# Optimization experiments

Measured on AMD Instinct MI355X. Metric: run time of the kernel, lower is better.

Reference implementation:

```python
import jax, jax.numpy as jnp
import numpy as np

N, E, D, H, DH = 10000, 160000, 1024, 4, 256  # nodes, edges, feat dim, heads, per-head dim
NB, G = 3, 64  # num_blocks, num graphs in batch
NEG_SLOPE = 0.2  # PyG GATConv default


def setup_inputs() -> dict:
    key = jax.random.key(0)
    ks = jax.random.split(key, 8)
    x = jax.random.normal(ks[0], (N, D), jnp.float32)
    edge_index = jax.random.randint(ks[1], (2, E), 0, N)
    batch = jnp.sort(jax.random.randint(ks[2], (N,), 0, G))
    W = jax.random.normal(ks[3], (NB, D, H * DH), jnp.float32) * 0.03
    a_src = jax.random.normal(ks[4], (NB, H, DH), jnp.float32) * 0.1
    a_dst = jax.random.normal(ks[5], (NB, H, DH), jnp.float32) * 0.1
    b = jnp.zeros((NB, H * DH), jnp.float32)
    Wr = jax.random.normal(ks[6], (D, 2), jnp.float32) * 0.03
    br = jnp.zeros((2,), jnp.float32)
    return dict(x=x, edge_index=edge_index, batch=batch, W=W, a_src=a_src,
                a_dst=a_dst, b=b, Wr=Wr, br=br)


def _gat_conv(x, src, dst, W, asrc, adst, bias):
    # Linear projection per head: [N, H, DH]
    h = (x @ W).reshape(N, H, DH)
    # Per-node attention logits (src/dst halves of the GAT attention vector)
    es = jnp.einsum('nhd,hd->nh', h, asrc)  # [N, H]
    ed = jnp.einsum('nhd,hd->nh', h, adst)  # [N, H]
    # Edge scores + LeakyReLU
    e = jax.nn.leaky_relu(es[src] + ed[dst], NEG_SLOPE)  # [Etot, H]
    # Segment softmax over edges sharing the same destination node
    m = jax.ops.segment_max(e, dst, num_segments=N)
    p = jnp.exp(e - m[dst])
    s = jax.ops.segment_sum(p, dst, num_segments=N)
    alpha = p / (s[dst] + 1e-16)  # [Etot, H]
    # Scatter-aggregate weighted source features
    out = jax.ops.segment_sum(h[src] * alpha[:, :, None], dst, num_segments=N)
    return out.reshape(N, H * DH) + bias


def reference(x, edge_index, batch, W, a_src, a_dst, b, Wr, br):
    # PyG GATConv adds self-loops by default
    loops = jnp.arange(N)
    src = jnp.concatenate([edge_index[0], loops])
    dst = jnp.concatenate([edge_index[1], loops])
    # Faithful to the source: each block reads the ORIGINAL x; dropout in eval mode.
    h = x
    for i in range(NB):
        h = jax.nn.relu(_gat_conv(x, src, dst, W[i], a_src[i], a_dst[i], b[i]))
    # global_mean_pool over graph assignment `batch`
    sums = jax.ops.segment_sum(h, batch, num_segments=G)
    cnt = jax.ops.segment_sum(jnp.ones((N, 1), h.dtype), batch, num_segments=G)
    pooled = sums / jnp.maximum(cnt, 1.0)
    return pooled @ Wr + br
```

## Files before the change

kernel.cpp:

```cpp
#include <hip/hip_runtime.h>
#include <hip/hip_bf16.h>

#define N_NODES 10000
#define N_EDGES 160000
#define ETOT    (N_NODES + N_EDGES)
#define DIM     1024
#define NHEAD   4
#define DHEAD   256
#define NGRAPH  64
#define NEG_SLOPE 0.2f

typedef short  bf16x8 __attribute__((ext_vector_type(8)));
typedef float  f32x4  __attribute__((ext_vector_type(4)));
typedef unsigned short u16x4 __attribute__((ext_vector_type(4)));

__device__ __forceinline__ unsigned short f2bf_rne(float v) {
    unsigned u = __builtin_bit_cast(unsigned, v);
    return (unsigned short)((u + 0x7fffu + ((u >> 16) & 1u)) >> 16);
}
__device__ __forceinline__ float bf2f(unsigned short b) {
    return __builtin_bit_cast(float, (unsigned)b << 16);
}
__device__ __forceinline__ float lrelu(float x) { return x > 0.f ? x : NEG_SLOPE * x; }

__global__ void zero_k(float* p, int n) {
    int i = blockIdx.x * 256 + threadIdx.x;
    if (i < n) p[i] = 0.f;
}

__global__ __launch_bounds__(256) void prep_x(const float* __restrict__ x,
                                              unsigned short* __restrict__ xhi,
                                              unsigned short* __restrict__ xlo) {
    int i = blockIdx.x * 256 + threadIdx.x;
    if ((size_t)i * 4 >= (size_t)N_NODES * DIM) return;
    f32x4 v = *(const f32x4*)(x + (size_t)i * 4);
    u16x4 hi, lo;
#pragma unroll
    for (int j = 0; j < 4; ++j) {
        unsigned short hb = f2bf_rne(v[j]);
        float r = v[j] - bf2f(hb);
        hi[j] = hb;
        lo[j] = f2bf_rne(r);
    }
    *(u16x4*)(xhi + (size_t)i * 4) = hi;
    *(u16x4*)(xlo + (size_t)i * 4) = lo;
}

__global__ __launch_bounds__(256) void prep_w(const float* __restrict__ W2,
                                              unsigned short* __restrict__ wthi,
                                              unsigned short* __restrict__ wtlo) {
    __shared__ float tile[64][65];
    int bc = blockIdx.x;
    int bk = blockIdx.y;
    int t = threadIdx.x;
    int tj = t & 63, ti = t >> 6;
#pragma unroll
    for (int u = 0; u < 16; ++u) {
        int r = u * 4 + ti;
        tile[r][tj] = W2[(size_t)(bk * 64 + r) * DIM + bc * 64 + tj];
    }
    __syncthreads();
#pragma unroll
    for (int u = 0; u < 16; ++u) {
        int cr = u * 4 + ti;
        float v = tile[tj][cr];
        unsigned short hb = f2bf_rne(v);
        float rres = v - bf2f(hb);
        size_t o = (size_t)(bc * 64 + cr) * DIM + bk * 64 + tj;
        wthi[o] = hb;
        wtlo[o] = f2bf_rne(rres);
    }
}

#define BM 128
#define BN 128
#define BK 32
#define LDK 40

__global__ __launch_bounds__(256) void gemm3(const unsigned short* __restrict__ xhi,
                                             const unsigned short* __restrict__ xlo,
                                             const unsigned short* __restrict__ wthi,
                                             const unsigned short* __restrict__ wtlo,
                                             float* __restrict__ hout) {
    __shared__ short lds[4][BM * LDK];
    const int t = threadIdx.x;
    const int r0 = blockIdx.y * BM;
    const int c0 = blockIdx.x * BN;
    const int lane = t & 63, wid = t >> 6;
    const int wm = wid >> 1, wn = wid & 1;

    f32x4 acc[4][4];
#pragma unroll
    for (int mi = 0; mi < 4; ++mi)
#pragma unroll
        for (int ni = 0; ni < 4; ++ni) acc[mi][ni] = (f32x4){0.f, 0.f, 0.f, 0.f};

    const int rL = lane & 15;
    const int koff = (lane >> 4) * 8;

    for (int k0 = 0; k0 < DIM; k0 += BK) {
        __syncthreads();
#pragma unroll
        for (int u = 0; u < 8; ++u) {
            int idx = u * 256 + t;
            int which = idx >> 9;
            int rem = idx & 511;
            int row = rem >> 2;
            int seg = rem & 3;
            const unsigned short* src;
            bool ok = true;
            if (which == 0)      { int gr = r0 + row; ok = gr < N_NODES; src = xhi + (size_t)gr * DIM + k0 + seg * 8; }
            else if (which == 1) { int gr = r0 + row; ok = gr < N_NODES; src = xlo + (size_t)gr * DIM + k0 + seg * 8; }
            else if (which == 2) { src = wthi + (size_t)(c0 + row) * DIM + k0 + seg * 8; }
            else                 { src = wtlo + (size_t)(c0 + row) * DIM + k0 + seg * 8; }
            bf16x8 v = {0,0,0,0,0,0,0,0};
            if (ok) v = *(const bf16x8*)src;
            *(bf16x8*)&lds[which][row * LDK + seg * 8] = v;
        }
        __syncthreads();

        bf16x8 ahi[4], alo[4], bhi[4], blo[4];
#pragma unroll
        for (int mi = 0; mi < 4; ++mi) {
            int row = wm * 64 + mi * 16 + rL;
            ahi[mi] = *(const bf16x8*)&lds[0][row * LDK + koff];
            alo[mi] = *(const bf16x8*)&lds[1][row * LDK + koff];
        }
#pragma unroll
        for (int ni = 0; ni < 4; ++ni) {
            int row = wn * 64 + ni * 16 + rL;
            bhi[ni] = *(const bf16x8*)&lds[2][row * LDK + koff];
            blo[ni] = *(const bf16x8*)&lds[3][row * LDK + koff];
        }
#pragma unroll
        for (int mi = 0; mi < 4; ++mi)
#pragma unroll
            for (int ni = 0; ni < 4; ++ni) {
                f32x4 c = acc[mi][ni];
                c = __builtin_amdgcn_mfma_f32_16x16x32_bf16(ahi[mi], bhi[ni], c, 0, 0, 0);
                c = __builtin_amdgcn_mfma_f32_16x16x32_bf16(ahi[mi], blo[ni], c, 0, 0, 0);
                c = __builtin_amdgcn_mfma_f32_16x16x32_bf16(alo[mi], bhi[ni], c, 0, 0, 0);
                acc[mi][ni] = c;
            }
    }

#pragma unroll
    for (int mi = 0; mi < 4; ++mi)
#pragma unroll
        for (int ni = 0; ni < 4; ++ni)
#pragma unroll
            for (int v = 0; v < 4; ++v) {
                int row = r0 + wm * 64 + mi * 16 + ((lane >> 4) << 2) + v;
                if (row < N_NODES) {
                    int col = c0 + wn * 64 + ni * 16 + (lane & 15);
                    hout[(size_t)row * DIM + col] = acc[mi][ni][v];
                }
            }
}

__global__ __launch_bounds__(256) void dots_k(const float* __restrict__ h,
                                              const float* __restrict__ asrc,
                                              const float* __restrict__ adst,
                                              float* __restrict__ es,
                                              float* __restrict__ ed) {
    int wid = threadIdx.x >> 6, lane = threadIdx.x & 63;
    int n = blockIdx.x * 4 + wid;
    if (n >= N_NODES) return;
    const float* hr = h + (size_t)n * DIM;
    f32x4 sa = {0.f, 0.f, 0.f, 0.f}, sd = {0.f, 0.f, 0.f, 0.f};
#pragma unroll
    for (int k = 0; k < 4; ++k)
#pragma unroll
        for (int j = 0; j < 4; ++j) {
            int col = k * 256 + j * 64 + lane;
            float v = hr[col];
            sa[k] += v * asrc[col];
            sd[k] += v * adst[col];
        }
#pragma unroll
    for (int d = 1; d < 64; d <<= 1) {
#pragma unroll
        for (int k = 0; k < 4; ++k) {
            sa[k] += __shfl_xor(sa[k], d);
            sd[k] += __shfl_xor(sd[k], d);
        }
    }
    if (lane == 0) {
        *(f32x4*)(es + (size_t)n * 4) = sa;
        *(f32x4*)(ed + (size_t)n * 4) = sd;
    }
}

__global__ void init_counts(const int* __restrict__ batch, int* cnt, int* cursor, int* gcnt) {
    int n = blockIdx.x * 256 + threadIdx.x;
    if (n >= N_NODES) return;
    cnt[n] = 1;
    cursor[n] = 0;
    atomicAdd(gcnt + batch[n], 1);
}

__global__ void edge_hist(const int* __restrict__ dst, int* cnt) {
    int e = blockIdx.x * 256 + threadIdx.x;
    if (e >= N_EDGES) return;
    atomicAdd(cnt + dst[e], 1);
}

__global__ __launch_bounds__(1024) void scan_k(const int* __restrict__ cnt, int* __restrict__ off) {
    __shared__ int s[1024];
    int t = threadIdx.x;
    int running = 0;
    for (int c0 = 0; c0 < N_NODES; c0 += 1024) {
        int i = c0 + t;
        int v = (i < N_NODES) ? cnt[i] : 0;
        s[t] = v;
        __syncthreads();
        for (int d = 1; d < 1024; d <<= 1) {
            int x = (t >= d) ? s[t - d] : 0;
            __syncthreads();
            s[t] += x;
            __syncthreads();
        }
        if (i < N_NODES) off[i] = running + s[t] - v;
        int tot = s[1023];
        __syncthreads();
        running += tot;
    }
}

__global__ void bucket_k(const int* __restrict__ src, const int* __restrict__ dst,
                         const int* __restrict__ off, int* cursor, int* bucket) {
    int e = blockIdx.x * 256 + threadIdx.x;
    if (e >= ETOT) return;
    int d = (e < N_EDGES) ? dst[e] : (e - N_EDGES);
    int pos = atomicAdd(cursor + d, 1);
    bucket[off[d] + pos] = e;
}

#define HCAP 192
__global__ __launch_bounds__(256) void aggregate_k(const float* __restrict__ h,
                                                   const float* __restrict__ es,
                                                   const float* __restrict__ ed,
                                                   const int* __restrict__ src,
                                                   const int* __restrict__ cnt,
                                                   const int* __restrict__ off,
                                                   const int* __restrict__ bucket,
                                                   const int* __restrict__ batch,
                                                   const float* __restrict__ b2,
                                                   float* __restrict__ pooled) {
    int n = blockIdx.x, t = threadIdx.x;
    int deg = cnt[n], base = off[n];
    f32x4 edn = *(const f32x4*)(ed + (size_t)n * 4);
    __shared__ int  s_src[HCAP];
    __shared__ f32x4 s_e[HCAP];
    __shared__ f32x4 wred[4];

    f32x4 m4 = {-3e38f, -3e38f, -3e38f, -3e38f};
    for (int i = t; i < deg; i += 256) {
        int eid = bucket[base + i];
        int s = (eid < N_EDGES) ? src[eid] : (eid - N_EDGES);
        f32x4 e4 = *(const f32x4*)(es + (size_t)s * 4);
        e4.x = lrelu(e4.x + edn.x); e4.y = lrelu(e4.y + edn.y);
        e4.z = lrelu(e4.z + edn.z); e4.w = lrelu(e4.w + edn.w);
        if (i < HCAP) { s_src[i] = s; s_e[i] = e4; }
        m4.x = fmaxf(m4.x, e4.x); m4.y = fmaxf(m4.y, e4.y);
        m4.z = fmaxf(m4.z, e4.z); m4.w = fmaxf(m4.w, e4.w);
    }
#pragma unroll
    for (int d = 1; d < 64; d <<= 1) {
        m4.x = fmaxf(m4.x, __shfl_xor(m4.x, d));
        m4.y = fmaxf(m4.y, __shfl_xor(m4.y, d));
        m4.z = fmaxf(m4.z, __shfl_xor(m4.z, d));
        m4.w = fmaxf(m4.w, __shfl_xor(m4.w, d));
    }
    if ((t & 63) == 0) wred[t >> 6] = m4;
    __syncthreads();
    f32x4 mm = wred[0];
#pragma unroll
    for (int w = 1; w < 4; ++w) {
        mm.x = fmaxf(mm.x, wred[w].x); mm.y = fmaxf(mm.y, wred[w].y);
        mm.z = fmaxf(mm.z, wred[w].z); mm.w = fmaxf(mm.w, wred[w].w);
    }
    int hd = t >> 6;
    float mh = hd == 0 ? mm.x : hd == 1 ? mm.y : hd == 2 ? mm.z : mm.w;

    f32x4 acc = {0.f, 0.f, 0.f, 0.f};
    float sump = 0.f;
    for (int i = 0; i < deg; ++i) {
        int s;
        f32x4 e4;
        if (i < HCAP) { s = s_src[i]; e4 = s_e[i]; }
        else {
            int eid = bucket[base + i];
            s = (eid < N_EDGES) ? src[eid] : (eid - N_EDGES);
            e4 = *(const f32x4*)(es + (size_t)s * 4);
            e4.x = lrelu(e4.x + edn.x); e4.y = lrelu(e4.y + edn.y);
            e4.z = lrelu(e4.z + edn.z); e4.w = lrelu(e4.w + edn.w);
        }
        float eh = hd == 0 ? e4.x : hd == 1 ? e4.y : hd == 2 ? e4.z : e4.w;
        float p = expf(eh - mh);
        sump += p;
        f32x4 hv = *(const f32x4*)(h + (size_t)s * DIM + t * 4);
        acc += p * hv;
    }
    float inv = 1.0f / (sump + 1e-16f);
    f32x4 bb = *(const f32x4*)(b2 + t * 4);
    f32x4 r = acc * inv + bb;
    r.x = fmaxf(r.x, 0.f); r.y = fmaxf(r.y, 0.f);
    r.z = fmaxf(r.z, 0.f); r.w = fmaxf(r.w, 0.f);
    int bg = batch[n];
    float* pp = pooled + (size_t)bg * DIM + t * 4;
    atomicAdd(pp + 0, r.x);
    atomicAdd(pp + 1, r.y);
    atomicAdd(pp + 2, r.z);
    atomicAdd(pp + 3, r.w);
}

__global__ __launch_bounds__(256) void final_k(const float* __restrict__ pooled,
                                               const int* __restrict__ gcnt,
                                               const float* __restrict__ Wr,
                                               const float* __restrict__ br,
                                               float* __restrict__ out) {
    int g = blockIdx.x, t = threadIdx.x;
    float s0 = 0.f, s1 = 0.f;
    for (int d = t; d < DIM; d += 256) {
        float v = pooled[(size_t)g * DIM + d];
        s0 += v * Wr[d * 2];
        s1 += v * Wr[d * 2 + 1];
    }
    __shared__ float r0[256], r1[256];
    r0[t] = s0; r1[t] = s1;
    __syncthreads();
    for (int st = 128; st > 0; st >>= 1) {
        if (t < st) { r0[t] += r0[t + st]; r1[t] += r1[t + st]; }
        __syncthreads();
    }
    if (t == 0) {
        float c = fmaxf((float)gcnt[g], 1.f);
        out[g * 2 + 0] = r0[0] / c + br[0];
        out[g * 2 + 1] = r1[0] / c + br[1];
    }
}

extern "C" void kernel_launch(void* const* d_in, const int* in_sizes, int n_in,
                              void* d_out, int out_size, void* d_ws, size_t ws_size,
                              hipStream_t stream) {
    (void)in_sizes; (void)n_in; (void)out_size;
    const float* x     = (const float*)d_in[0];
    const int*   ei    = (const int*)d_in[1];
    const int*   batch = (const int*)d_in[2];
    const float* W     = (const float*)d_in[3];
    const float* a_src = (const float*)d_in[4];
    const float* a_dst = (const float*)d_in[5];
    const float* b     = (const float*)d_in[6];
    const float* Wr    = (const float*)d_in[7];
    const float* br    = (const float*)d_in[8];

    const float* W2    = W + (size_t)2 * DIM * DIM;
    const float* asrc2 = a_src + 2 * NHEAD * DHEAD;
    const float* adst2 = a_dst + 2 * NHEAD * DHEAD;
    const float* b2    = b + 2 * DIM;
    const int* srcI = ei;
    const int* dstI = ei + N_EDGES;

    char* wsp = (char*)d_ws;
    size_t o = 0;
    auto alloc = [&](size_t bytes) -> char* {
        char* p = wsp + o;
        o = (o + bytes + 255) & ~(size_t)255;
        return p;
    };
    unsigned short* xhi  = (unsigned short*)alloc((size_t)N_NODES * DIM * 2);
    unsigned short* xlo  = (unsigned short*)alloc((size_t)N_NODES * DIM * 2);
    unsigned short* wthi = (unsigned short*)alloc((size_t)DIM * DIM * 2);
    unsigned short* wtlo = (unsigned short*)alloc((size_t)DIM * DIM * 2);
    float* h    = (float*)alloc((size_t)N_NODES * DIM * 4);
    float* es   = (float*)alloc((size_t)N_NODES * 4 * 4);
    float* ed   = (float*)alloc((size_t)N_NODES * 4 * 4);
    int*   cnt  = (int*)alloc((size_t)N_NODES * 4);
    int*   offs = (int*)alloc((size_t)N_NODES * 4);
    int*   curs = (int*)alloc((size_t)N_NODES * 4);
    int*   bkt  = (int*)alloc((size_t)ETOT * 4);
    float* pooled = (float*)alloc((size_t)NGRAPH * DIM * 4);
    int*   gcnt   = (int*)alloc(256);
    (void)ws_size;

    const int ZN = NGRAPH * DIM + 64;
    zero_k<<<(ZN + 255) / 256, 256, 0, stream>>>(pooled, ZN);

    prep_x<<<(N_NODES * DIM / 4 + 255) / 256, 256, 0, stream>>>(x, xhi, xlo);
    prep_w<<<dim3(16, 16), 256, 0, stream>>>(W2, wthi, wtlo);
    gemm3<<<dim3(DIM / BN, (N_NODES + BM - 1) / BM), 256, 0, stream>>>(xhi, xlo, wthi, wtlo, h);
    dots_k<<<(N_NODES + 3) / 4, 256, 0, stream>>>(h, asrc2, adst2, es, ed);

    init_counts<<<(N_NODES + 255) / 256, 256, 0, stream>>>(batch, cnt, curs, gcnt);
    edge_hist<<<(N_EDGES + 255) / 256, 256, 0, stream>>>(dstI, cnt);
    scan_k<<<1, 1024, 0, stream>>>(cnt, offs);
    bucket_k<<<(ETOT + 255) / 256, 256, 0, stream>>>(srcI, dstI, offs, curs, bkt);

    aggregate_k<<<N_NODES, 256, 0, stream>>>(h, es, ed, srcI, cnt, offs, bkt, batch, b2, pooled);
    final_k<<<NGRAPH, 256, 0, stream>>>(pooled, gcnt, Wr, br, (float*)d_out);
}
```

Measured before the change: 478.4 us.

## Store projected features as bf16, use direct-to-LDS loads, replace atomic pooling

The GEMM output h is now written as bf16, which halves its footprint for the GEMM store, the dots kernel and the edge-gather reads in aggregation, at the cost of bf16 rounding on features. The GEMM tile loads switch to global_load_lds with one wave per operand, and the LDS padding is dropped, which may bring bank conflicts. The wave-shuffle scan and the vectorized dots kernel cut synchronisation. The per-element float atomics into pooled are replaced by a dense per-node output (aliased onto xhi) followed by a contiguous-range pool kernel, which relies on batch being sorted.

```diff
diff --git a/kernel.cpp b/kernel.cpp
--- a/kernel.cpp
+++ b/kernel.cpp
@@ -13,6 +13,7 @@
 typedef short  bf16x8 __attribute__((ext_vector_type(8)));
 typedef float  f32x4  __attribute__((ext_vector_type(4)));
 typedef unsigned short u16x4 __attribute__((ext_vector_type(4)));
+typedef unsigned short u16x8 __attribute__((ext_vector_type(8)));
 
 __device__ __forceinline__ unsigned short f2bf_rne(float v) {
     unsigned u = __builtin_bit_cast(unsigned, v);
@@ -22,11 +23,6 @@
     return __builtin_bit_cast(float, (unsigned)b << 16);
 }
 __device__ __forceinline__ float lrelu(float x) { return x > 0.f ? x : NEG_SLOPE * x; }
-
-__global__ void zero_k(float* p, int n) {
-    int i = blockIdx.x * 256 + threadIdx.x;
-    if (i < n) p[i] = 0.f;
-}
 
 __global__ __launch_bounds__(256) void prep_x(const float* __restrict__ x,
                                               unsigned short* __restrict__ xhi,
@@ -75,20 +71,23 @@
 #define BM 128
 #define BN 128
 #define BK 32
-#define LDK 40
 
 __global__ __launch_bounds__(256) void gemm3(const unsigned short* __restrict__ xhi,
                                              const unsigned short* __restrict__ xlo,
                                              const unsigned short* __restrict__ wthi,
                                              const unsigned short* __restrict__ wtlo,
-                                             float* __restrict__ hout) {
-    __shared__ short lds[4][BM * LDK];
+                                             unsigned short* __restrict__ hb) {
+    __shared__ short lds[4][BM * BK];
     const int t = threadIdx.x;
     const int r0 = blockIdx.y * BM;
     const int c0 = blockIdx.x * BN;
     const int lane = t & 63, wid = t >> 6;
     const int wm = wid >> 1, wn = wid & 1;
 
+    const unsigned short* const srcs[4] = {xhi, xlo, wthi, wtlo};
+    const unsigned short* wbase = srcs[wid];
+    const int rowb = (wid < 2) ? r0 : c0;
+
     f32x4 acc[4][4];
 #pragma unroll
     for (int mi = 0; mi < 4; ++mi)
@@ -101,21 +100,13 @@
     for (int k0 = 0; k0 < DIM; k0 += BK) {
         __syncthreads();
 #pragma unroll
-        for (int u = 0; u < 8; ++u) {
-            int idx = u * 256 + t;
-            int which = idx >> 9;
-            int rem = idx & 511;
-            int row = rem >> 2;
-            int seg = rem & 3;
-            const unsigned short* src;
-            bool ok = true;
-            if (which == 0)      { int gr = r0 + row; ok = gr < N_NODES; src = xhi + (size_t)gr * DIM + k0 + seg * 8; }
-            else if (which == 1) { int gr = r0 + row; ok = gr < N_NODES; src = xlo + (size_t)gr * DIM + k0 + seg * 8; }
-            else if (which == 2) { src = wthi + (size_t)(c0 + row) * DIM + k0 + seg * 8; }
-            else                 { src = wtlo + (size_t)(c0 + row) * DIM + k0 + seg * 8; }
-            bf16x8 v = {0,0,0,0,0,0,0,0};
-            if (ok) v = *(const bf16x8*)src;
-            *(bf16x8*)&lds[which][row * LDK + seg * 8] = v;
+        for (int j = 0; j < 8; ++j) {
+            const unsigned short* g = wbase
+                + (size_t)(rowb + j * 16 + (lane >> 2)) * DIM + k0 + (lane & 3) * 8;
+            __builtin_amdgcn_global_load_lds(
+                (const __attribute__((address_space(1))) unsigned int*)g,
+                (__attribute__((address_space(3))) unsigned int*)&lds[wid][j * 512],
+                16, 0, 0);
         }
         __syncthreads();
 
@@ -123,14 +114,14 @@
 #pragma unroll
         for (int mi = 0; mi < 4; ++mi) {
             int row = wm * 64 + mi * 16 + rL;
-            ahi[mi] = *(const bf16x8*)&lds[0][row * LDK + koff];
-            alo[mi] = *(const bf16x8*)&lds[1][row * LDK + koff];
+            ahi[mi] = *(const bf16x8*)&lds[0][row * BK + koff];
+            alo[mi] = *(const bf16x8*)&lds[1][row * BK + koff];
         }
 #pragma unroll
         for (int ni = 0; ni < 4; ++ni) {
             int row = wn * 64 + ni * 16 + rL;
-            bhi[ni] = *(const bf16x8*)&lds[2][row * LDK + koff];
-            blo[ni] = *(const bf16x8*)&lds[3][row * LDK + koff];
+            bhi[ni] = *(const bf16x8*)&lds[2][row * BK + koff];
+            blo[ni] = *(const bf16x8*)&lds[3][row * BK + koff];
         }
 #pragma unroll
         for (int mi = 0; mi < 4; ++mi)
@@ -153,12 +144,12 @@
                 int row = r0 + wm * 64 + mi * 16 + ((lane >> 4) << 2) + v;
                 if (row < N_NODES) {
                     int col = c0 + wn * 64 + ni * 16 + (lane & 15);
-                    hout[(size_t)row * DIM + col] = acc[mi][ni][v];
+                    hb[(size_t)row * DIM + col] = f2bf_rne(acc[mi][ni][v]);
                 }
             }
 }
 
-__global__ __launch_bounds__(256) void dots_k(const float* __restrict__ h,
+__global__ __launch_bounds__(256) void dots_k(const unsigned short* __restrict__ hb,
                                               const float* __restrict__ asrc,
                                               const float* __restrict__ adst,
                                               float* __restrict__ es,
@@ -166,37 +157,51 @@
     int wid = threadIdx.x >> 6, lane = threadIdx.x & 63;
     int n = blockIdx.x * 4 + wid;
     if (n >= N_NODES) return;
-    const float* hr = h + (size_t)n * DIM;
-    f32x4 sa = {0.f, 0.f, 0.f, 0.f}, sd = {0.f, 0.f, 0.f, 0.f};
-#pragma unroll
-    for (int k = 0; k < 4; ++k)
-#pragma unroll
-        for (int j = 0; j < 4; ++j) {
-            int col = k * 256 + j * 64 + lane;
-            float v = hr[col];
-            sa[k] += v * asrc[col];
-            sd[k] += v * adst[col];
-        }
-#pragma unroll
-    for (int d = 1; d < 64; d <<= 1) {
-#pragma unroll
-        for (int k = 0; k < 4; ++k) {
-            sa[k] += __shfl_xor(sa[k], d);
-            sd[k] += __shfl_xor(sd[k], d);
-        }
-    }
-    if (lane == 0) {
-        *(f32x4*)(es + (size_t)n * 4) = sa;
-        *(f32x4*)(ed + (size_t)n * 4) = sd;
-    }
-}
-
-__global__ void init_counts(const int* __restrict__ batch, int* cnt, int* cursor, int* gcnt) {
+    const unsigned short* hr = hb + (size_t)n * DIM + lane * 16;
+    u16x8 a = *(const u16x8*)hr;
+    u16x8 b8 = *(const u16x8*)(hr + 8);
+    const float* ap = asrc + lane * 16;
+    const float* dp = adst + lane * 16;
+    float sa = 0.f, sd = 0.f;
+#pragma unroll
+    for (int j = 0; j < 8; ++j) {
+        float v = bf2f(a[j]);
+        sa += v * ap[j];
+        sd += v * dp[j];
+    }
+#pragma unroll
+    for (int j = 0; j < 8; ++j) {
+        float v = bf2f(b8[j]);
+        sa += v * ap[8 + j];
+        sd += v * dp[8 + j];
+    }
+#pragma unroll
+    for (int d = 1; d < 16; d <<= 1) {
+        sa += __shfl_xor(sa, d);
+        sd += __shfl_xor(sd, d);
+    }
+    if ((lane & 15) == 0) {
+        int head = lane >> 4;
+        es[(size_t)n * 4 + head] = sa;
+        ed[(size_t)n * 4 + head] = sd;
+    }
+}
+
+__global__ void init_misc(int* gcnt, int* gbeg, int* gend) {
+    int t = threadIdx.x;
+    if (t < NGRAPH) { gcnt[t] = 0; gbeg[t] = 0x7fffffff; gend[t] = -1; }
+}
+
+__global__ void init_counts(const int* __restrict__ batch, int* cnt, int* cursor,
+                            int* gcnt, int* gbeg, int* gend) {
     int n = blockIdx.x * 256 + threadIdx.x;
     if (n >= N_NODES) return;
     cnt[n] = 1;
     cursor[n] = 0;
-    atomicAdd(gcnt + batch[n], 1);
+    int b = batch[n];
+    atomicAdd(gcnt + b, 1);
+    atomicMin(gbeg + b, n);
+    atomicMax(gend + b, n);
 }
 
 __global__ void edge_hist(const int* __restrict__ dst, int* cnt) {
@@ -206,24 +211,35 @@
 }
 
 __global__ __launch_bounds__(1024) void scan_k(const int* __restrict__ cnt, int* __restrict__ off) {
-    __shared__ int s[1024];
-    int t = threadIdx.x;
+    __shared__ int wsh[16];
+    __shared__ int tot_s;
+    int t = threadIdx.x, lane = t & 63, wv = t >> 6;
     int running = 0;
     for (int c0 = 0; c0 < N_NODES; c0 += 1024) {
         int i = c0 + t;
         int v = (i < N_NODES) ? cnt[i] : 0;
-        s[t] = v;
+        int s = v;
+#pragma unroll
+        for (int d = 1; d < 64; d <<= 1) {
+            int y = __shfl_up(s, d);
+            if (lane >= d) s += y;
+        }
+        if (lane == 63) wsh[wv] = s;
         __syncthreads();
-        for (int d = 1; d < 1024; d <<= 1) {
-            int x = (t >= d) ? s[t - d] : 0;
-            __syncthreads();
-            s[t] += x;
-            __syncthreads();
-        }
-        if (i < N_NODES) off[i] = running + s[t] - v;
-        int tot = s[1023];
+        if (wv == 0) {
+            int wsv = (lane < 16) ? wsh[lane] : 0;
+            int e = wsv;
+#pragma unroll
+            for (int d = 1; d < 16; d <<= 1) {
+                int y = __shfl_up(e, d);
+                if (lane >= d) e += y;
+            }
+            if (lane < 16) wsh[lane] = e - wsv;
+            if (lane == 15) tot_s = e;
+        }
         __syncthreads();
-        running += tot;
+        if (i < N_NODES) off[i] = running + wsh[wv] + s - v;
+        running += tot_s;
     }
 }
 
@@ -237,16 +253,15 @@
 }
 
 #define HCAP 192
-__global__ __launch_bounds__(256) void aggregate_k(const float* __restrict__ h,
+__global__ __launch_bounds__(256) void aggregate_k(const unsigned short* __restrict__ hb,
                                                    const float* __restrict__ es,
                                                    const float* __restrict__ ed,
                                                    const int* __restrict__ src,
                                                    const int* __restrict__ cnt,
                                                    const int* __restrict__ off,
                                                    const int* __restrict__ bucket,
-                                                   const int* __restrict__ batch,
                                                    const float* __restrict__ b2,
-                                                   float* __restrict__ pooled) {
+                                                   float* __restrict__ out) {
     int n = blockIdx.x, t = threadIdx.x;
     int deg = cnt[n], base = off[n];
     f32x4 edn = *(const f32x4*)(ed + (size_t)n * 4);
@@ -299,7 +314,8 @@
         float eh = hd == 0 ? e4.x : hd == 1 ? e4.y : hd == 2 ? e4.z : e4.w;
         float p = expf(eh - mh);
         sump += p;
-        f32x4 hv = *(const f32x4*)(h + (size_t)s * DIM + t * 4);
+        u16x4 q = *(const u16x4*)(hb + (size_t)s * DIM + t * 4);
+        f32x4 hv = {bf2f(q[0]), bf2f(q[1]), bf2f(q[2]), bf2f(q[3])};
         acc += p * hv;
     }
     float inv = 1.0f / (sump + 1e-16f);
@@ -307,12 +323,19 @@
     f32x4 r = acc * inv + bb;
     r.x = fmaxf(r.x, 0.f); r.y = fmaxf(r.y, 0.f);
     r.z = fmaxf(r.z, 0.f); r.w = fmaxf(r.w, 0.f);
-    int bg = batch[n];
-    float* pp = pooled + (size_t)bg * DIM + t * 4;
-    atomicAdd(pp + 0, r.x);
-    atomicAdd(pp + 1, r.y);
-    atomicAdd(pp + 2, r.z);
-    atomicAdd(pp + 3, r.w);
+    *(f32x4*)(out + (size_t)n * DIM + t * 4) = r;
+}
+
+__global__ __launch_bounds__(256) void pool_k(const float* __restrict__ out,
+                                              const int* __restrict__ gbeg,
+                                              const int* __restrict__ gend,
+                                              float* __restrict__ pooled) {
+    int g = blockIdx.x, c = blockIdx.y, t = threadIdx.x;
+    int col = c * 256 + t;
+    int b0 = gbeg[g], b1 = gend[g];
+    float acc = 0.f;
+    for (int n = b0; n <= b1; ++n) acc += out[(size_t)n * DIM + col];
+    pooled[(size_t)g * DIM + col] = acc;
 }
 
 __global__ __launch_bounds__(256) void final_k(const float* __restrict__ pooled,
@@ -344,7 +367,7 @@
 extern "C" void kernel_launch(void* const* d_in, const int* in_sizes, int n_in,
                               void* d_out, int out_size, void* d_ws, size_t ws_size,
                               hipStream_t stream) {
-    (void)in_sizes; (void)n_in; (void)out_size;
+    (void)in_sizes; (void)n_in; (void)out_size; (void)ws_size;
     const float* x     = (const float*)d_in[0];
     const int*   ei    = (const int*)d_in[1];
     const int*   batch = (const int*)d_in[2];
@@ -373,7 +396,7 @@
     unsigned short* xlo  = (unsigned short*)alloc((size_t)N_NODES * DIM * 2);
     unsigned short* wthi = (unsigned short*)alloc((size_t)DIM * DIM * 2);
     unsigned short* wtlo = (unsigned short*)alloc((size_t)DIM * DIM * 2);
-    float* h    = (float*)alloc((size_t)N_NODES * DIM * 4);
+    unsigned short* hb   = (unsigned short*)alloc((size_t)N_NODES * DIM * 2);
     float* es   = (float*)alloc((size_t)N_NODES * 4 * 4);
     float* ed   = (float*)alloc((size_t)N_NODES * 4 * 4);
     int*   cnt  = (int*)alloc((size_t)N_NODES * 4);
@@ -381,22 +404,23 @@
     int*   curs = (int*)alloc((size_t)N_NODES * 4);
     int*   bkt  = (int*)alloc((size_t)ETOT * 4);
     float* pooled = (float*)alloc((size_t)NGRAPH * DIM * 4);
-    int*   gcnt   = (int*)alloc(256);
-    (void)ws_size;
-
-    const int ZN = NGRAPH * DIM + 64;
-    zero_k<<<(ZN + 255) / 256, 256, 0, stream>>>(pooled, ZN);
-
+    int*   gcnt   = (int*)alloc(NGRAPH * 4);
+    int*   gbeg   = (int*)alloc(NGRAPH * 4);
+    int*   gend   = (int*)alloc(NGRAPH * 4);
+    float* outn = (float*)xhi;
+
+    init_misc<<<1, 64, 0, stream>>>(gcnt, gbeg, gend);
     prep_x<<<(N_NODES * DIM / 4 + 255) / 256, 256, 0, stream>>>(x, xhi, xlo);
     prep_w<<<dim3(16, 16), 256, 0, stream>>>(W2, wthi, wtlo);
-    gemm3<<<dim3(DIM / BN, (N_NODES + BM - 1) / BM), 256, 0, stream>>>(xhi, xlo, wthi, wtlo, h);
-    dots_k<<<(N_NODES + 3) / 4, 256, 0, stream>>>(h, asrc2, adst2, es, ed);
-
-    init_counts<<<(N_NODES + 255) / 256, 256, 0, stream>>>(batch, cnt, curs, gcnt);
+    gemm3<<<dim3(DIM / BN, (N_NODES + BM - 1) / BM), 256, 0, stream>>>(xhi, xlo, wthi, wtlo, hb);
+    dots_k<<<(N_NODES + 3) / 4, 256, 0, stream>>>(hb, asrc2, adst2, es, ed);
+
+    init_counts<<<(N_NODES + 255) / 256, 256, 0, stream>>>(batch, cnt, curs, gcnt, gbeg, gend);
     edge_hist<<<(N_EDGES + 255) / 256, 256, 0, stream>>>(dstI, cnt);
     scan_k<<<1, 1024, 0, stream>>>(cnt, offs);
     bucket_k<<<(ETOT + 255) / 256, 256, 0, stream>>>(srcI, dstI, offs, curs, bkt);
 
-    aggregate_k<<<N_NODES, 256, 0, stream>>>(h, es, ed, srcI, cnt, offs, bkt, batch, b2, pooled);
+    aggregate_k<<<N_NODES, 256, 0, stream>>>(hb, es, ed, srcI, cnt, offs, bkt, b2, outn);
+    pool_k<<<dim3(NGRAPH, 4), 256, 0, stream>>>(outn, gbeg, gend, pooled);
     final_k<<<NGRAPH, 256, 0, stream>>>(pooled, gcnt, Wr, br, (float*)d_out);
 }
```

Measured after the change: 400.3 us. 16.3% less time.
